# Performance work log

Measured on AMD Instinct MI355X. Metric: run time of the kernel, lower is better.

The kernel has to match this reference:

```python
import jax, jax.numpy as jnp
import jax.scipy as jsp
import numpy as np

NUM_EMBEDDINGS = 256
EMBEDDING_DIM = 64
SPARSITY_LEVEL = 4
N_BINS = 16
COEF_MAX = 3.0
COEF_MU = 50.0
COMMITMENT_COST = 0.25
EPSILON = 1e-10


def _normalize_dict(dictionary):
    # F.normalize(dict, p=2, dim=0, eps): x / max(||x||_2, eps) per column
    nrm = jnp.linalg.norm(dictionary, axis=0, keepdims=True)
    return dictionary / jnp.maximum(nrm, EPSILON)


def _quantize_coeff_mu_law(coeff):
    inv_log1p_mu = 1.0 / np.log1p(COEF_MU)  # scalar constant
    c = jnp.clip(coeff, -COEF_MAX, COEF_MAX) / COEF_MAX
    encoded = jnp.sign(c) * jnp.log1p(jnp.abs(c) * COEF_MU) * inv_log1p_mu
    scaled = (encoded + 1.0) * ((N_BINS - 1) / 2.0)
    bin_idx = jnp.clip(jnp.round(scaled).astype(jnp.int32), 0, N_BINS - 1)
    # dequantize
    z = bin_idx.astype(coeff.dtype) * (2.0 / (N_BINS - 1)) - 1.0
    decoded = jnp.sign(z) * (jnp.expm1(jnp.abs(z) / inv_log1p_mu) / COEF_MU) * COEF_MAX
    return bin_idx, decoded


def batch_omp_with_support(X, Dn, K):
    # X: [M, Bs] signals, Dn: [M, N] normalized dictionary
    G = Dn.T @ Dn                       # [N, N] Gram
    h_bar = (Dn.T @ X).T                # [Bs, N] correlations
    Bs, N = h_bar.shape
    dt = h_bar.dtype
    h = h_bar
    mask = jnp.zeros((Bs, N), dtype=bool)
    L = jnp.ones((Bs, 1, 1), dtype=dt)  # incremental Cholesky of G[I, I]
    I = jnp.zeros((Bs, 0), dtype=jnp.int32)
    x_sel = jnp.zeros((Bs, 0), dtype=dt)
    rows = jnp.arange(Bs)
    for k in range(1, K + 1):  # K is small & static -> unrolled
        idx = jnp.argmax(jnp.abs(h) * (~mask), axis=1).astype(jnp.int32)
        mask = mask.at[rows, idx].set(True)
        if k > 1:
            G_stack = G[I, idx[:, None]]                     # [Bs, k-1]
            w = jsp.linalg.solve_triangular(L, G_stack[..., None], lower=True)  # [Bs,k-1,1]
            wT = jnp.swapaxes(w, 1, 2)                       # [Bs,1,k-1]
            w_corner = jnp.sqrt(jnp.clip(1.0 - jnp.sum(wT * wT, axis=2, keepdims=True), 1e-12))
            top = jnp.concatenate([L, jnp.zeros((Bs, k - 1, 1), dt)], axis=2)
            bot = jnp.concatenate([wT, w_corner], axis=2)
            L = jnp.concatenate([top, bot], axis=1)          # [Bs,k,k]
        I = jnp.concatenate([I, idx[:, None]], axis=1)       # [Bs,k]
        h_stack = jnp.take_along_axis(h_bar, I, axis=1)[..., None]  # [Bs,k,1]
        # cholesky_solve: L L^T x = h
        y = jsp.linalg.solve_triangular(L, h_stack, lower=True)
        xs = jsp.linalg.solve_triangular(jnp.swapaxes(L, 1, 2), y, lower=False)
        x_sel = xs[..., 0]                                   # [Bs,k] coeffs aligned w/ support
        beta = jnp.einsum('bk,bkn->bn', x_sel, G[I])         # [Bs,N]
        h = h_bar - beta
    return I, x_sel


def setup_inputs() -> dict:
    key = jax.random.key(0)
    k1, k2 = jax.random.split(key)
    z_e = jax.random.normal(k1, (32, EMBEDDING_DIM, 64, 64), dtype=jnp.float32)
    dictionary = jax.random.normal(k2, (EMBEDDING_DIM, NUM_EMBEDDINGS), dtype=jnp.float32) * 0.02
    return {"z_e": z_e, "dictionary": dictionary}


def reference(z_e, dictionary):
    B, C, H, W = z_e.shape
    Dn = _normalize_dict(dictionary)
    signals = jnp.transpose(z_e, (0, 2, 3, 1)).reshape(-1, C).T  # [C, B*H*W]
    # OMP runs with no grad (torch.no_grad in original)
    support, coeffs = jax.lax.stop_gradient(
        batch_omp_with_support(jax.lax.stop_gradient(signals), jax.lax.stop_gradient(Dn), SPARSITY_LEVEL)
    )
    # mu-law quantize coefficients (constants w.r.t. grads)
    bin_idx, coeffs_q = _quantize_coeff_mu_law(coeffs)
    # reconstruct with quantized coeffs; dictionary path is differentiable
    atoms = Dn.T[support]                                    # [Bs, K, C]
    recon_flat = jnp.einsum('bkc,bk->bc', atoms, coeffs_q)
    recon = jnp.transpose(recon_flat.reshape(B, H, W, C), (0, 3, 1, 2))
    # VQ-VAE style losses + STE
    e_latent_loss = jnp.mean((jax.lax.stop_gradient(recon) - z_e) ** 2)
    q_latent_loss = jnp.mean((recon - jax.lax.stop_gradient(z_e)) ** 2)
    loss = q_latent_loss + COMMITMENT_COST * e_latent_loss
    z_q = z_e + jax.lax.stop_gradient(recon - z_e)
    return z_q, loss


if __name__ == '__main__':
    out = reference(**setup_inputs())
    print(out[0].shape, out[1])
```

## Files before the change

kernel.cpp:

```cpp
#include <hip/hip_runtime.h>
#include <math.h>

#define NEMB 256
#define DIM 64
#define SIGS_B 64
#define THREADS 256
#define NSIG 131072
#define GRID (NSIG / SIGS_B)

#define LOG1P50 3.9318256327243257
#define INV_MU_F ((float)(1.0 / LOG1P50))
#define TWO15_F ((float)(2.0 / 15.0))

#define LB_SIG   0
#define LB_XS    16384
#define LB_QI    17408
#define LB_RED   18432
#define LDS_BYTES 18464

typedef float f2 __attribute__((ext_vector_type(2)));

__device__ __forceinline__ float rdlane_f(float v, int lane)
{
    return __builtin_bit_cast(float, __builtin_amdgcn_readlane(__builtin_bit_cast(int, v), lane));
}

template<int CTRL>
__device__ __forceinline__ float dpp_fmax(float m)
{
    int sh = __builtin_amdgcn_update_dpp(0, __builtin_bit_cast(int, m), CTRL, 0xf, 0xf, true);
    return fmaxf(m, __builtin_bit_cast(float, sh));
}

__device__ __forceinline__ float wave_max_nn(float v)
{
    v = dpp_fmax<0x111>(v);
    v = dpp_fmax<0x112>(v);
    v = dpp_fmax<0x114>(v);
    v = dpp_fmax<0x118>(v);
    v = dpp_fmax<0x142>(v);
    v = dpp_fmax<0x143>(v);
    return v;
}

__global__ void k_ng(const float* __restrict__ D, float* __restrict__ Dn,
                     float* __restrict__ G,
                     double* __restrict__ loss_acc, unsigned int* __restrict__ ctr)
{
#pragma clang fp contract(off)
    __shared__ float nrmS[NEMB];
    __shared__ float coli[DIM];
    int i = blockIdx.x, j = threadIdx.x;
    if (i == 0 && j == 0) { loss_acc[0] = 0.0; ctr[0] = 0u; }
    float ss = 0.0f;
    for (int c = 0; c < DIM; c++) {
        float v = D[c * NEMB + j];
        float sq = v * v;
        ss = ss + sq;
    }
    float nrm = fmaxf(sqrtf(ss), 1e-10f);
    nrmS[j] = nrm;
    __syncthreads();
    if (j < DIM) {
        float dni = D[j * NEMB + i] / nrmS[i];
        coli[j] = dni;
        Dn[j * NEMB + i] = dni;
    }
    __syncthreads();
    float s = 0.0f;
#pragma unroll 8
    for (int c = 0; c < DIM; c++) {
        float dnj = D[c * NEMB + j] / nrm;
        s = fmaf(coli[c], dnj, s);
    }
    G[i * NEMB + j] = s;
}

__device__ __forceinline__ float quant_decode(float coeff)
{
#pragma clang fp contract(off)
    float c = fminf(fmaxf(coeff, -3.0f), 3.0f) / 3.0f;
    float ac = fabsf(c);
    float sgn = (c > 0.0f) ? 1.0f : ((c < 0.0f) ? -1.0f : 0.0f);
    float l = log1pf(ac * 50.0f);
    float enc = (sgn * l) * INV_MU_F;
    float scaled = (enc + 1.0f) * 7.5f;
    int bin = (int)rintf(scaled);
    bin = bin < 0 ? 0 : (bin > 15 ? 15 : bin);
    float t = (float)bin * TWO15_F;
    float zv = t - 1.0f;
    float az = fabsf(zv);
    float sz = (zv > 0.0f) ? 1.0f : ((zv < 0.0f) ? -1.0f : 0.0f);
    float e = expm1f(az / INV_MU_F);
    return (sz * (e / 50.0f)) * 3.0f;
}

__device__ __forceinline__ void omp_pair(const f2* hbA_in, const f2* hbB_in,
                                         int lane, int hi,
                                         const float* __restrict__ G,
                                         float* __restrict__ xsv,
                                         int* __restrict__ qi, int sA)
{
#pragma clang fp contract(off)
    f2 hbsiA[2] = {hbA_in[0], hbA_in[1]};
    f2 hbsiB[2] = {hbB_in[0], hbB_in[1]};
    f2 hA[2] = {hbsiA[0], hbsiA[1]};
    f2 hB[2] = {hbsiB[0], hbsiB[1]};
    f2 GrA[3][2], GrB[3][2];
    float Lm[4][4];
    int IvA[4], IvB[4];
    float y[4], xs[4];
    int m4A = 0, m4B = 0;
#pragma unroll
    for (int kk = 0; kk < 4; kk++) {
        float bvA = -1.0f, bvB = -1.0f;
        int bjA = 0, bjB = 0;
#pragma unroll
        for (int j = 0; j < 4; j++) {
            float vA_ = (m4A & (1 << j)) ? 0.0f : fabsf(hA[j >> 1][j & 1]);
            if (vA_ > bvA) { bvA = vA_; bjA = j; }
            float vB_ = (m4B & (1 << j)) ? 0.0f : fabsf(hB[j >> 1][j & 1]);
            if (vB_ > bvB) { bvB = vB_; bjB = j; }
        }
        float mA = wave_max_nn(bvA);
        float mB = wave_max_nn(bvB);
        float vmaxA = rdlane_f(mA, 63);
        float vmaxB = rdlane_f(mB, 63);
        unsigned long long ballA = __ballot(bvA == vmaxA);
        unsigned long long ballB = __ballot(bvB == vmaxB);
        int ownerA = __ffsll((long long)ballA) - 1;
        int ownerB = __ffsll((long long)ballB) - 1;
        int bjAo = __builtin_amdgcn_readlane(bjA, ownerA);
        int bjBo = __builtin_amdgcn_readlane(bjB, ownerB);
        int idxA = 4 * ownerA + bjAo;
        int idxB = 4 * ownerB + bjBo;
        m4A |= (lane == ownerA) ? (1 << bjAo) : 0;
        m4B |= (lane == ownerB) ? (1 << bjBo) : 0;
        IvA[kk] = idxA; IvB[kk] = idxB;
        float tvA = hbsiA[0][0];
        tvA = (bjA == 1) ? hbsiA[0][1] : tvA;
        tvA = (bjA == 2) ? hbsiA[1][0] : tvA;
        tvA = (bjA == 3) ? hbsiA[1][1] : tvA;
        float tvB = hbsiB[0][0];
        tvB = (bjB == 1) ? hbsiB[0][1] : tvB;
        tvB = (bjB == 2) ? hbsiB[1][0] : tvB;
        tvB = (bjB == 3) ? hbsiB[1][1] : tvB;
        float hselA = rdlane_f(tvA, ownerA);
        float hselB = rdlane_f(tvB, ownerB);
        float hsel = hi ? hselB : hselA;
        if (kk < 3) {
            const float4 ga = *(const float4*)(G + ((size_t)idxA << 8) + 4 * lane);
            const float4 gb = *(const float4*)(G + ((size_t)idxB << 8) + 4 * lane);
            GrA[kk][0].x = ga.x; GrA[kk][0].y = ga.y;
            GrA[kk][1].x = ga.z; GrA[kk][1].y = ga.w;
            GrB[kk][0].x = gb.x; GrB[kk][0].y = gb.y;
            GrB[kk][1].x = gb.z; GrB[kk][1].y = gb.w;
        }
        if (kk > 0) {
            float Gs[3], w[3];
#pragma unroll
            for (int j = 0; j < 3; j++)
                if (j < kk) {
                    float eA = GrA[j][0][0];
                    eA = (bjAo == 1) ? GrA[j][0][1] : eA;
                    eA = (bjAo == 2) ? GrA[j][1][0] : eA;
                    eA = (bjAo == 3) ? GrA[j][1][1] : eA;
                    float eB = GrB[j][0][0];
                    eB = (bjBo == 1) ? GrB[j][0][1] : eB;
                    eB = (bjBo == 2) ? GrB[j][1][0] : eB;
                    eB = (bjBo == 3) ? GrB[j][1][1] : eB;
                    float gA = rdlane_f(eA, ownerA);
                    float gB = rdlane_f(eB, ownerB);
                    Gs[j] = hi ? gB : gA;
                }
#pragma unroll
            for (int r = 0; r < 3; r++) {
                if (r < kk) {
                    float acc = 0.0f;
#pragma unroll
                    for (int cc = 0; cc < 3; cc++)
                        if (cc < r) { float p = Lm[r][cc] * w[cc]; acc = acc + p; }
                    float t2 = Gs[r] - acc;
                    w[r] = (r == 0) ? t2 : t2 / Lm[r][r];
                }
            }
            float ssum = 0.0f;
#pragma unroll
            for (int j = 0; j < 3; j++)
                if (j < kk) { float p = w[j] * w[j]; ssum = ssum + p; }
            float om = 1.0f - ssum;
            float wc = sqrtf(fmaxf(om, 1e-12f));
#pragma unroll
            for (int cc = 0; cc < 3; cc++)
                if (cc < kk) Lm[kk][cc] = w[cc];
            Lm[kk][kk] = wc;
        } else {
            Lm[0][0] = 1.0f;
        }
        {
            float acc = 0.0f;
#pragma unroll
            for (int cc = 0; cc < 3; cc++)
                if (cc < kk) { float p = Lm[kk][cc] * y[cc]; acc = acc + p; }
            float t2 = hsel - acc;
            y[kk] = (kk == 0) ? t2 : t2 / Lm[kk][kk];
        }
#pragma unroll
        for (int r = 3; r >= 0; r--) {
            if (r <= kk) {
                float acc = 0.0f;
#pragma unroll
                for (int cc = 0; cc < 4; cc++)
                    if (cc > r && cc <= kk) { float p = Lm[cc][r] * xs[cc]; acc = acc + p; }
                float t2 = y[r] - acc;
                xs[r] = (r == 0) ? t2 : t2 / Lm[r][r];
            }
        }
        if (kk < 3) {
            float xsA[4], xsB[4];
#pragma unroll
            for (int j = 0; j < 4; j++)
                if (j <= kk) {
                    xsA[j] = rdlane_f(xs[j], 0);
                    xsB[j] = rdlane_f(xs[j], 32);
                }
#pragma unroll
            for (int jp = 0; jp < 2; jp++) {
                f2 bsA = {0.0f, 0.0f};
                f2 bsB = {0.0f, 0.0f};
#pragma unroll
                for (int jj = 0; jj < 3; jj++)
                    if (jj <= kk) {
                        f2 xa = {xsA[jj], xsA[jj]};
                        f2 xb = {xsB[jj], xsB[jj]};
                        f2 pA = xa * GrA[jj][jp];
                        bsA = bsA + pA;
                        f2 pB = xb * GrB[jj][jp];
                        bsB = bsB + pB;
                    }
                hA[jp] = hbsiA[jp] - bsA;
                hB[jp] = hbsiB[jp] - bsB;
            }
        }
    }
    if ((lane & 31) == 0) {
        int s = sA + hi;
#pragma unroll
        for (int j = 0; j < 4; j++) {
            xsv[j * SIGS_B + s] = xs[j];
            qi[j * SIGS_B + s] = hi ? IvB[j] : IvA[j];
        }
    }
}

__launch_bounds__(THREADS, 4)
__global__ void k_omp(const float* __restrict__ z,
                      const float* __restrict__ Dn_g,
                      const float* __restrict__ G,
                      double* __restrict__ loss_acc,
                      unsigned int* __restrict__ ctr,
                      float* __restrict__ zq,
                      float* __restrict__ loss_out)
{
    extern __shared__ char smem[];
    float* sig = (float*)(smem + LB_SIG);
    float* xsv = (float*)(smem + LB_XS);
    int* qi = (int*)(smem + LB_QI);
    double* red = (double*)(smem + LB_RED);

    int tid = threadIdx.x;
    int lane = tid & 63;
    int hi = lane >> 5;
    int wid = tid >> 6;

    long sbase = (long)blockIdx.x * SIGS_B;
    int b = (int)(sbase >> 12);
    int pl0 = (int)(sbase & 4095);
    const float* zb = z + ((size_t)b << 18) + pl0;
    {
        int w = tid & (SIGS_B - 1);
        int g = tid >> 6;
#pragma unroll
        for (int i = 0; i < 16; i++) {
            int c = g * 16 + i;
            sig[c * SIGS_B + w] = zb[(size_t)c * 4096 + w];
        }
    }
    __syncthreads();

    for (int g2 = 0; g2 < 2; g2++) {
        int s0 = wid * 16 + g2 * 8;
        f2 hb[8][2];
#pragma unroll
        for (int a = 0; a < 8; a++) {
            hb[a][0] = (f2){0.0f, 0.0f};
            hb[a][1] = (f2){0.0f, 0.0f};
        }
#pragma unroll 8
        for (int c = 0; c < DIM; c++) {
            float4 sva = *(const float4*)(sig + c * SIGS_B + s0);
            float4 svb = *(const float4*)(sig + c * SIGS_B + s0 + 4);
            float s8[8] = {sva.x, sva.y, sva.z, sva.w, svb.x, svb.y, svb.z, svb.w};
            float4 dv = *(const float4*)(Dn_g + c * NEMB + 4 * lane);
            f2 d0; d0.x = dv.x; d0.y = dv.y;
            f2 d1; d1.x = dv.z; d1.y = dv.w;
#pragma unroll
            for (int a = 0; a < 8; a++) {
                f2 sa = {s8[a], s8[a]};
                hb[a][0] = __builtin_elementwise_fma(sa, d0, hb[a][0]);
                hb[a][1] = __builtin_elementwise_fma(sa, d1, hb[a][1]);
            }
        }
#pragma unroll
        for (int p = 0; p < 4; p++)
            omp_pair(hb[2 * p], hb[2 * p + 1], lane, hi, G, xsv, qi, s0 + 2 * p);
    }
    __syncthreads();

    {
        int jq = tid >> 6;
        int wq = tid & (SIGS_B - 1);
        xsv[jq * SIGS_B + wq] = quant_decode(xsv[jq * SIGS_B + wq]);
    }
    __syncthreads();

    double lsum = 0.0;
    float* zqb = zq + ((size_t)b << 18) + pl0;
    {
#pragma clang fp contract(off)
        int w = tid & (SIGS_B - 1);
        int g = tid >> 6;
        float q0 = xsv[0 * SIGS_B + w], q1 = xsv[1 * SIGS_B + w];
        float q2 = xsv[2 * SIGS_B + w], q3 = xsv[3 * SIGS_B + w];
        int i0 = qi[0 * SIGS_B + w], i1 = qi[1 * SIGS_B + w];
        int i2 = qi[2 * SIGS_B + w], i3 = qi[3 * SIGS_B + w];
#pragma unroll
        for (int ci = 0; ci < 16; ci++) {
            int c = g * 16 + ci;
            const float* dr = Dn_g + c * NEMB;
            float p0 = q0 * dr[i0];
            float p1 = q1 * dr[i1];
            float p2 = q2 * dr[i2];
            float p3 = q3 * dr[i3];
            float r = p0 + p1;
            r = r + p2;
            r = r + p3;
            float zev = sig[c * SIGS_B + w];
            float d = r - zev;
            float zqv = zev + d;
            lsum += (double)d * (double)d;
            zqb[(size_t)c * 4096 + w] = zqv;
        }
    }
#pragma unroll
    for (int off = 32; off > 0; off >>= 1) lsum += __shfl_xor(lsum, off);
    if (lane == 0) red[wid] = lsum;
    __syncthreads();
    if (tid == 0) {
        double t = 0.0;
#pragma unroll
        for (int i = 0; i < 4; i++) t += red[i];
        atomicAdd(loss_acc, t);
        __threadfence();
        unsigned int done = atomicAdd(ctr, 1u);
        if (done == GRID - 1) {
            double m = atomicAdd(loss_acc, 0.0) / 8388608.0;
            loss_out[0] = (float)(m + 0.25 * m);
        }
    }
}

extern "C" void kernel_launch(void* const* d_in, const int* in_sizes, int n_in,
                              void* d_out, int out_size, void* d_ws, size_t ws_size,
                              hipStream_t stream)
{
    const float* z = (const float*)d_in[0];
    const float* D = (const float*)d_in[1];
    float* out = (float*)d_out;
    char* ws = (char*)d_ws;
    double* loss_acc = (double*)ws;
    unsigned int* ctr = (unsigned int*)(ws + 8);
    float* Dn = (float*)(ws + 256);
    float* G = (float*)(ws + 256 + 65536);

    k_ng<<<NEMB, NEMB, 0, stream>>>(D, Dn, G, loss_acc, ctr);
    hipFuncSetAttribute(reinterpret_cast<const void*>(k_omp),
                        hipFuncAttributeMaxDynamicSharedMemorySize, LDS_BYTES);
    k_omp<<<GRID, THREADS, LDS_BYTES, stream>>>(z, Dn, G, loss_acc, ctr, out, out + 8388608);
    (void)in_sizes; (void)n_in; (void)out_size; (void)ws_size;
}
```

Before: 309.3 us.

## Run OMP on four signals per wave and gather reconstruction atoms from transposed dictionary

The OMP solve now processes four signals per wavefront, one per 16-lane quarter, instead of two per half-wave. The Cholesky update is written out with scalar registers, and the Gram entries it needs are read directly from global memory instead of being extracted from cached Gram rows with lane reads. The reconstruction step now reads atoms from a new transposed dictionary copy with float4 loads instead of strided scalar gathers. In exchange, the code carries more live registers and more redundant Gram row loads per iteration, which could hurt occupancy.

```diff
diff --git a/kernel.cpp b/kernel.cpp
--- a/kernel.cpp
+++ b/kernel.cpp
@@ -44,7 +44,7 @@
 }
 
 __global__ void k_ng(const float* __restrict__ D, float* __restrict__ Dn,
-                     float* __restrict__ G,
+                     float* __restrict__ DnT, float* __restrict__ G,
                      double* __restrict__ loss_acc, unsigned int* __restrict__ ctr)
 {
 #pragma clang fp contract(off)
@@ -65,6 +65,7 @@
         float dni = D[j * NEMB + i] / nrmS[i];
         coli[j] = dni;
         Dn[j * NEMB + i] = dni;
+        DnT[i * DIM + j] = dni;
     }
     __syncthreads();
     float s = 0.0f;
@@ -95,167 +96,238 @@
     return (sz * (e / 50.0f)) * 3.0f;
 }
 
-__device__ __forceinline__ void omp_pair(const f2* hbA_in, const f2* hbB_in,
-                                         int lane, int hi,
+__device__ __forceinline__ void omp_quad(const f2 (*hbsi)[2], int lane, int qt,
                                          const float* __restrict__ G,
                                          float* __restrict__ xsv,
-                                         int* __restrict__ qi, int sA)
+                                         int* __restrict__ qi, int s0)
 {
 #pragma clang fp contract(off)
-    f2 hbsiA[2] = {hbA_in[0], hbA_in[1]};
-    f2 hbsiB[2] = {hbB_in[0], hbB_in[1]};
-    f2 hA[2] = {hbsiA[0], hbsiA[1]};
-    f2 hB[2] = {hbsiB[0], hbsiB[1]};
-    f2 GrA[3][2], GrB[3][2];
-    float Lm[4][4];
-    int IvA[4], IvB[4];
-    float y[4], xs[4];
-    int m4A = 0, m4B = 0;
+    f2 h0[2] = {hbsi[0][0], hbsi[0][1]};
+    f2 h1[2] = {hbsi[1][0], hbsi[1][1]};
+    f2 h2[2] = {hbsi[2][0], hbsi[2][1]};
+    f2 h3[2] = {hbsi[3][0], hbsi[3][1]};
+    int m40 = 0, m41 = 0, m42 = 0, m43 = 0;
+    int Iv0[4], Iv1[4], Iv2[4], Iv3[4];
+    int Ivq[4];
+    float L10, L11, L20, L21, L22, L30, L31, L32, L33;
+    float y0, y1, y2, y3;
+    float x0 = 0.f, x1 = 0.f, x2 = 0.f, x3 = 0.f;
 #pragma unroll
     for (int kk = 0; kk < 4; kk++) {
-        float bvA = -1.0f, bvB = -1.0f;
-        int bjA = 0, bjB = 0;
+        float bv0 = -1.f, bv1 = -1.f, bv2 = -1.f, bv3 = -1.f;
+        int bj0 = 0, bj1 = 0, bj2 = 0, bj3 = 0;
 #pragma unroll
         for (int j = 0; j < 4; j++) {
-            float vA_ = (m4A & (1 << j)) ? 0.0f : fabsf(hA[j >> 1][j & 1]);
-            if (vA_ > bvA) { bvA = vA_; bjA = j; }
-            float vB_ = (m4B & (1 << j)) ? 0.0f : fabsf(hB[j >> 1][j & 1]);
-            if (vB_ > bvB) { bvB = vB_; bjB = j; }
-        }
-        float mA = wave_max_nn(bvA);
-        float mB = wave_max_nn(bvB);
-        float vmaxA = rdlane_f(mA, 63);
-        float vmaxB = rdlane_f(mB, 63);
-        unsigned long long ballA = __ballot(bvA == vmaxA);
-        unsigned long long ballB = __ballot(bvB == vmaxB);
-        int ownerA = __ffsll((long long)ballA) - 1;
-        int ownerB = __ffsll((long long)ballB) - 1;
-        int bjAo = __builtin_amdgcn_readlane(bjA, ownerA);
-        int bjBo = __builtin_amdgcn_readlane(bjB, ownerB);
-        int idxA = 4 * ownerA + bjAo;
-        int idxB = 4 * ownerB + bjBo;
-        m4A |= (lane == ownerA) ? (1 << bjAo) : 0;
-        m4B |= (lane == ownerB) ? (1 << bjBo) : 0;
-        IvA[kk] = idxA; IvB[kk] = idxB;
-        float tvA = hbsiA[0][0];
-        tvA = (bjA == 1) ? hbsiA[0][1] : tvA;
-        tvA = (bjA == 2) ? hbsiA[1][0] : tvA;
-        tvA = (bjA == 3) ? hbsiA[1][1] : tvA;
-        float tvB = hbsiB[0][0];
-        tvB = (bjB == 1) ? hbsiB[0][1] : tvB;
-        tvB = (bjB == 2) ? hbsiB[1][0] : tvB;
-        tvB = (bjB == 3) ? hbsiB[1][1] : tvB;
-        float hselA = rdlane_f(tvA, ownerA);
-        float hselB = rdlane_f(tvB, ownerB);
-        float hsel = hi ? hselB : hselA;
+            float a0 = (m40 & (1 << j)) ? 0.f : fabsf(h0[j >> 1][j & 1]);
+            if (a0 > bv0) { bv0 = a0; bj0 = j; }
+            float a1 = (m41 & (1 << j)) ? 0.f : fabsf(h1[j >> 1][j & 1]);
+            if (a1 > bv1) { bv1 = a1; bj1 = j; }
+            float a2 = (m42 & (1 << j)) ? 0.f : fabsf(h2[j >> 1][j & 1]);
+            if (a2 > bv2) { bv2 = a2; bj2 = j; }
+            float a3 = (m43 & (1 << j)) ? 0.f : fabsf(h3[j >> 1][j & 1]);
+            if (a3 > bv3) { bv3 = a3; bj3 = j; }
+        }
+        float r0 = wave_max_nn(bv0);
+        float r1 = wave_max_nn(bv1);
+        float r2 = wave_max_nn(bv2);
+        float r3 = wave_max_nn(bv3);
+        float vm0 = rdlane_f(r0, 63), vm1 = rdlane_f(r1, 63);
+        float vm2 = rdlane_f(r2, 63), vm3 = rdlane_f(r3, 63);
+        unsigned long long bl0 = __ballot(bv0 == vm0);
+        unsigned long long bl1 = __ballot(bv1 == vm1);
+        unsigned long long bl2 = __ballot(bv2 == vm2);
+        unsigned long long bl3 = __ballot(bv3 == vm3);
+        int ow0 = __ffsll((long long)bl0) - 1;
+        int ow1 = __ffsll((long long)bl1) - 1;
+        int ow2 = __ffsll((long long)bl2) - 1;
+        int ow3 = __ffsll((long long)bl3) - 1;
+        int bo0 = __builtin_amdgcn_readlane(bj0, ow0);
+        int bo1 = __builtin_amdgcn_readlane(bj1, ow1);
+        int bo2 = __builtin_amdgcn_readlane(bj2, ow2);
+        int bo3 = __builtin_amdgcn_readlane(bj3, ow3);
+        int id0 = 4 * ow0 + bo0;
+        int id1 = 4 * ow1 + bo1;
+        int id2 = 4 * ow2 + bo2;
+        int id3 = 4 * ow3 + bo3;
+        m40 |= (lane == ow0) ? (1 << bo0) : 0;
+        m41 |= (lane == ow1) ? (1 << bo1) : 0;
+        m42 |= (lane == ow2) ? (1 << bo2) : 0;
+        m43 |= (lane == ow3) ? (1 << bo3) : 0;
+        float tv0 = hbsi[0][0][0];
+        tv0 = (bj0 == 1) ? hbsi[0][0][1] : tv0;
+        tv0 = (bj0 == 2) ? hbsi[0][1][0] : tv0;
+        tv0 = (bj0 == 3) ? hbsi[0][1][1] : tv0;
+        float tv1 = hbsi[1][0][0];
+        tv1 = (bj1 == 1) ? hbsi[1][0][1] : tv1;
+        tv1 = (bj1 == 2) ? hbsi[1][1][0] : tv1;
+        tv1 = (bj1 == 3) ? hbsi[1][1][1] : tv1;
+        float tv2 = hbsi[2][0][0];
+        tv2 = (bj2 == 1) ? hbsi[2][0][1] : tv2;
+        tv2 = (bj2 == 2) ? hbsi[2][1][0] : tv2;
+        tv2 = (bj2 == 3) ? hbsi[2][1][1] : tv2;
+        float tv3 = hbsi[3][0][0];
+        tv3 = (bj3 == 1) ? hbsi[3][0][1] : tv3;
+        tv3 = (bj3 == 2) ? hbsi[3][1][0] : tv3;
+        tv3 = (bj3 == 3) ? hbsi[3][1][1] : tv3;
+        float hs0 = rdlane_f(tv0, ow0);
+        float hs1 = rdlane_f(tv1, ow1);
+        float hs2 = rdlane_f(tv2, ow2);
+        float hs3 = rdlane_f(tv3, ow3);
+        Iv0[kk] = id0; Iv1[kk] = id1; Iv2[kk] = id2; Iv3[kk] = id3;
+        float hsel = (qt & 2) ? ((qt & 1) ? hs3 : hs2) : ((qt & 1) ? hs1 : hs0);
+        int idxq = (qt & 2) ? ((qt & 1) ? id3 : id2) : ((qt & 1) ? id1 : id0);
+        Ivq[kk] = idxq;
+        float Gs0 = 0.f, Gs1 = 0.f, Gs2 = 0.f;
+        if (kk > 0) Gs0 = G[(size_t)(Ivq[0] << 8) + idxq];
+        if (kk > 1) Gs1 = G[(size_t)(Ivq[1] << 8) + idxq];
+        if (kk > 2) Gs2 = G[(size_t)(Ivq[2] << 8) + idxq];
+        if (kk == 1) {
+            float cw0 = Gs0;
+            float css = cw0 * cw0;
+            float om = 1.0f - css;
+            L10 = cw0;
+            L11 = sqrtf(fmaxf(om, 1e-12f));
+        }
+        if (kk == 2) {
+            float cw0 = Gs0;
+            float ct = Gs1 - L10 * cw0;
+            float cw1 = ct / L11;
+            float css = cw0 * cw0;
+            float cp = cw1 * cw1; css = css + cp;
+            float om = 1.0f - css;
+            L20 = cw0; L21 = cw1;
+            L22 = sqrtf(fmaxf(om, 1e-12f));
+        }
+        if (kk == 3) {
+            float cw0 = Gs0;
+            float ct = Gs1 - L10 * cw0;
+            float cw1 = ct / L11;
+            float ca = L20 * cw0;
+            float cp = L21 * cw1; ca = ca + cp;
+            float ct3 = Gs2 - ca;
+            float cw2 = ct3 / L22;
+            float css = cw0 * cw0;
+            cp = cw1 * cw1; css = css + cp;
+            cp = cw2 * cw2; css = css + cp;
+            float om = 1.0f - css;
+            L30 = cw0; L31 = cw1; L32 = cw2;
+            L33 = sqrtf(fmaxf(om, 1e-12f));
+        }
+        if (kk == 0) y0 = hsel;
+        if (kk == 1) { float a = L10 * y0; y1 = (hsel - a) / L11; }
+        if (kk == 2) { float a = L20 * y0; float p = L21 * y1; a = a + p;
+                       y2 = (hsel - a) / L22; }
+        if (kk == 3) { float a = L30 * y0; float p = L31 * y1; a = a + p;
+                       p = L32 * y2; a = a + p;
+                       y3 = (hsel - a) / L33; }
+        if (kk == 0) { x0 = y0; }
+        if (kk == 1) {
+            x1 = y1 / L11;
+            float a = L10 * x1;
+            x0 = y0 - a;
+        }
+        if (kk == 2) {
+            x2 = y2 / L22;
+            float a = L21 * x2;
+            x1 = (y1 - a) / L11;
+            a = L10 * x1;
+            float p = L20 * x2; a = a + p;
+            x0 = y0 - a;
+        }
+        if (kk == 3) {
+            x3 = y3 / L33;
+            float a = L32 * x3;
+            x2 = (y2 - a) / L22;
+            a = L21 * x2;
+            float p = L31 * x3; a = a + p;
+            x1 = (y1 - a) / L11;
+            a = L10 * x1;
+            p = L20 * x2; a = a + p;
+            p = L30 * x3; a = a + p;
+            x0 = y0 - a;
+        }
         if (kk < 3) {
-            const float4 ga = *(const float4*)(G + ((size_t)idxA << 8) + 4 * lane);
-            const float4 gb = *(const float4*)(G + ((size_t)idxB << 8) + 4 * lane);
-            GrA[kk][0].x = ga.x; GrA[kk][0].y = ga.y;
-            GrA[kk][1].x = ga.z; GrA[kk][1].y = ga.w;
-            GrB[kk][0].x = gb.x; GrB[kk][0].y = gb.y;
-            GrB[kk][1].x = gb.z; GrB[kk][1].y = gb.w;
-        }
-        if (kk > 0) {
-            float Gs[3], w[3];
-#pragma unroll
-            for (int j = 0; j < 3; j++)
-                if (j < kk) {
-                    float eA = GrA[j][0][0];
-                    eA = (bjAo == 1) ? GrA[j][0][1] : eA;
-                    eA = (bjAo == 2) ? GrA[j][1][0] : eA;
-                    eA = (bjAo == 3) ? GrA[j][1][1] : eA;
-                    float eB = GrB[j][0][0];
-                    eB = (bjBo == 1) ? GrB[j][0][1] : eB;
-                    eB = (bjBo == 2) ? GrB[j][1][0] : eB;
-                    eB = (bjBo == 3) ? GrB[j][1][1] : eB;
-                    float gA = rdlane_f(eA, ownerA);
-                    float gB = rdlane_f(eB, ownerB);
-                    Gs[j] = hi ? gB : gA;
-                }
-#pragma unroll
-            for (int r = 0; r < 3; r++) {
-                if (r < kk) {
-                    float acc = 0.0f;
-#pragma unroll
-                    for (int cc = 0; cc < 3; cc++)
-                        if (cc < r) { float p = Lm[r][cc] * w[cc]; acc = acc + p; }
-                    float t2 = Gs[r] - acc;
-                    w[r] = (r == 0) ? t2 : t2 / Lm[r][r];
-                }
-            }
-            float ssum = 0.0f;
-#pragma unroll
-            for (int j = 0; j < 3; j++)
-                if (j < kk) { float p = w[j] * w[j]; ssum = ssum + p; }
-            float om = 1.0f - ssum;
-            float wc = sqrtf(fmaxf(om, 1e-12f));
-#pragma unroll
-            for (int cc = 0; cc < 3; cc++)
-                if (cc < kk) Lm[kk][cc] = w[cc];
-            Lm[kk][kk] = wc;
-        } else {
-            Lm[0][0] = 1.0f;
-        }
-        {
-            float acc = 0.0f;
-#pragma unroll
-            for (int cc = 0; cc < 3; cc++)
-                if (cc < kk) { float p = Lm[kk][cc] * y[cc]; acc = acc + p; }
-            float t2 = hsel - acc;
-            y[kk] = (kk == 0) ? t2 : t2 / Lm[kk][kk];
-        }
-#pragma unroll
-        for (int r = 3; r >= 0; r--) {
-            if (r <= kk) {
-                float acc = 0.0f;
-#pragma unroll
-                for (int cc = 0; cc < 4; cc++)
-                    if (cc > r && cc <= kk) { float p = Lm[cc][r] * xs[cc]; acc = acc + p; }
-                float t2 = y[r] - acc;
-                xs[r] = (r == 0) ? t2 : t2 / Lm[r][r];
-            }
-        }
-        if (kk < 3) {
-            float xsA[4], xsB[4];
-#pragma unroll
-            for (int j = 0; j < 4; j++)
-                if (j <= kk) {
-                    xsA[j] = rdlane_f(xs[j], 0);
-                    xsB[j] = rdlane_f(xs[j], 32);
-                }
-#pragma unroll
-            for (int jp = 0; jp < 2; jp++) {
-                f2 bsA = {0.0f, 0.0f};
-                f2 bsB = {0.0f, 0.0f};
-#pragma unroll
-                for (int jj = 0; jj < 3; jj++)
-                    if (jj <= kk) {
-                        f2 xa = {xsA[jj], xsA[jj]};
-                        f2 xb = {xsB[jj], xsB[jj]};
-                        f2 pA = xa * GrA[jj][jp];
-                        bsA = bsA + pA;
-                        f2 pB = xb * GrB[jj][jp];
-                        bsB = bsB + pB;
-                    }
-                hA[jp] = hbsiA[jp] - bsA;
-                hB[jp] = hbsiB[jp] - bsB;
-            }
-        }
-    }
-    if ((lane & 31) == 0) {
-        int s = sA + hi;
-#pragma unroll
-        for (int j = 0; j < 4; j++) {
-            xsv[j * SIGS_B + s] = xs[j];
-            qi[j * SIGS_B + s] = hi ? IvB[j] : IvA[j];
-        }
+            float xb00 = rdlane_f(x0, 0),  xb10 = rdlane_f(x0, 16);
+            float xb20 = rdlane_f(x0, 32), xb30 = rdlane_f(x0, 48);
+            float xb01 = 0.f, xb11 = 0.f, xb21 = 0.f, xb31 = 0.f;
+            float xb02 = 0.f, xb12 = 0.f, xb22 = 0.f, xb32 = 0.f;
+            if (kk > 0) { xb01 = rdlane_f(x1, 0);  xb11 = rdlane_f(x1, 16);
+                          xb21 = rdlane_f(x1, 32); xb31 = rdlane_f(x1, 48); }
+            if (kk > 1) { xb02 = rdlane_f(x2, 0);  xb12 = rdlane_f(x2, 16);
+                          xb22 = rdlane_f(x2, 32); xb32 = rdlane_f(x2, 48); }
+            const int l4 = 4 * lane;
+            float4 R00 = *(const float4*)(G + ((size_t)Iv0[0] << 8) + l4);
+            float4 R10 = *(const float4*)(G + ((size_t)Iv1[0] << 8) + l4);
+            float4 R20 = *(const float4*)(G + ((size_t)Iv2[0] << 8) + l4);
+            float4 R30 = *(const float4*)(G + ((size_t)Iv3[0] << 8) + l4);
+            float4 R01, R11, R21, R31, R02, R12, R22, R32;
+            if (kk > 0) {
+                R01 = *(const float4*)(G + ((size_t)Iv0[1] << 8) + l4);
+                R11 = *(const float4*)(G + ((size_t)Iv1[1] << 8) + l4);
+                R21 = *(const float4*)(G + ((size_t)Iv2[1] << 8) + l4);
+                R31 = *(const float4*)(G + ((size_t)Iv3[1] << 8) + l4);
+            }
+            if (kk > 1) {
+                R02 = *(const float4*)(G + ((size_t)Iv0[2] << 8) + l4);
+                R12 = *(const float4*)(G + ((size_t)Iv1[2] << 8) + l4);
+                R22 = *(const float4*)(G + ((size_t)Iv2[2] << 8) + l4);
+                R32 = *(const float4*)(G + ((size_t)Iv3[2] << 8) + l4);
+            }
+            {
+                f2 bsa = (f2){xb00, xb00} * (f2){R00.x, R00.y};
+                f2 bsb = (f2){xb00, xb00} * (f2){R00.z, R00.w};
+                if (kk > 0) { f2 pa = (f2){xb01, xb01} * (f2){R01.x, R01.y}; bsa = bsa + pa;
+                              f2 pb = (f2){xb01, xb01} * (f2){R01.z, R01.w}; bsb = bsb + pb; }
+                if (kk > 1) { f2 pa = (f2){xb02, xb02} * (f2){R02.x, R02.y}; bsa = bsa + pa;
+                              f2 pb = (f2){xb02, xb02} * (f2){R02.z, R02.w}; bsb = bsb + pb; }
+                h0[0] = hbsi[0][0] - bsa;
+                h0[1] = hbsi[0][1] - bsb;
+            }
+            {
+                f2 bsa = (f2){xb10, xb10} * (f2){R10.x, R10.y};
+                f2 bsb = (f2){xb10, xb10} * (f2){R10.z, R10.w};
+                if (kk > 0) { f2 pa = (f2){xb11, xb11} * (f2){R11.x, R11.y}; bsa = bsa + pa;
+                              f2 pb = (f2){xb11, xb11} * (f2){R11.z, R11.w}; bsb = bsb + pb; }
+                if (kk > 1) { f2 pa = (f2){xb12, xb12} * (f2){R12.x, R12.y}; bsa = bsa + pa;
+                              f2 pb = (f2){xb12, xb12} * (f2){R12.z, R12.w}; bsb = bsb + pb; }
+                h1[0] = hbsi[1][0] - bsa;
+                h1[1] = hbsi[1][1] - bsb;
+            }
+            {
+                f2 bsa = (f2){xb20, xb20} * (f2){R20.x, R20.y};
+                f2 bsb = (f2){xb20, xb20} * (f2){R20.z, R20.w};
+                if (kk > 0) { f2 pa = (f2){xb21, xb21} * (f2){R21.x, R21.y}; bsa = bsa + pa;
+                              f2 pb = (f2){xb21, xb21} * (f2){R21.z, R21.w}; bsb = bsb + pb; }
+                if (kk > 1) { f2 pa = (f2){xb22, xb22} * (f2){R22.x, R22.y}; bsa = bsa + pa;
+                              f2 pb = (f2){xb22, xb22} * (f2){R22.z, R22.w}; bsb = bsb + pb; }
+                h2[0] = hbsi[2][0] - bsa;
+                h2[1] = hbsi[2][1] - bsb;
+            }
+            {
+                f2 bsa = (f2){xb30, xb30} * (f2){R30.x, R30.y};
+                f2 bsb = (f2){xb30, xb30} * (f2){R30.z, R30.w};
+                if (kk > 0) { f2 pa = (f2){xb31, xb31} * (f2){R31.x, R31.y}; bsa = bsa + pa;
+                              f2 pb = (f2){xb31, xb31} * (f2){R31.z, R31.w}; bsb = bsb + pb; }
+                if (kk > 1) { f2 pa = (f2){xb32, xb32} * (f2){R32.x, R32.y}; bsa = bsa + pa;
+                              f2 pb = (f2){xb32, xb32} * (f2){R32.z, R32.w}; bsb = bsb + pb; }
+                h3[0] = hbsi[3][0] - bsa;
+                h3[1] = hbsi[3][1] - bsb;
+            }
+        }
+    }
+    if ((lane & 15) == 0) {
+        int s = s0 + qt;
+        xsv[0 * SIGS_B + s] = x0; xsv[1 * SIGS_B + s] = x1;
+        xsv[2 * SIGS_B + s] = x2; xsv[3 * SIGS_B + s] = x3;
+        qi[0 * SIGS_B + s] = Ivq[0]; qi[1 * SIGS_B + s] = Ivq[1];
+        qi[2 * SIGS_B + s] = Ivq[2]; qi[3 * SIGS_B + s] = Ivq[3];
     }
 }
 
 __launch_bounds__(THREADS, 4)
 __global__ void k_omp(const float* __restrict__ z,
                       const float* __restrict__ Dn_g,
+                      const float* __restrict__ DnT_g,
                       const float* __restrict__ G,
                       double* __restrict__ loss_acc,
                       unsigned int* __restrict__ ctr,
@@ -270,7 +342,7 @@
 
     int tid = threadIdx.x;
     int lane = tid & 63;
-    int hi = lane >> 5;
+    int qt = lane >> 4;
     int wid = tid >> 6;
 
     long sbase = (long)blockIdx.x * SIGS_B;
@@ -311,9 +383,8 @@
                 hb[a][1] = __builtin_elementwise_fma(sa, d1, hb[a][1]);
             }
         }
-#pragma unroll
-        for (int p = 0; p < 4; p++)
-            omp_pair(hb[2 * p], hb[2 * p + 1], lane, hi, G, xsv, qi, s0 + 2 * p);
+        omp_quad(hb,     lane, qt, G, xsv, qi, s0);
+        omp_quad(hb + 4, lane, qt, G, xsv, qi, s0 + 4);
     }
     __syncthreads();
 
@@ -334,22 +405,36 @@
         float q2 = xsv[2 * SIGS_B + w], q3 = xsv[3 * SIGS_B + w];
         int i0 = qi[0 * SIGS_B + w], i1 = qi[1 * SIGS_B + w];
         int i2 = qi[2 * SIGS_B + w], i3 = qi[3 * SIGS_B + w];
-#pragma unroll
-        for (int ci = 0; ci < 16; ci++) {
-            int c = g * 16 + ci;
-            const float* dr = Dn_g + c * NEMB;
-            float p0 = q0 * dr[i0];
-            float p1 = q1 * dr[i1];
-            float p2 = q2 * dr[i2];
-            float p3 = q3 * dr[i3];
-            float r = p0 + p1;
-            r = r + p2;
-            r = r + p3;
-            float zev = sig[c * SIGS_B + w];
-            float d = r - zev;
-            float zqv = zev + d;
-            lsum += (double)d * (double)d;
-            zqb[(size_t)c * 4096 + w] = zqv;
+        const float* t0p = DnT_g + (i0 << 6) + (g << 4);
+        const float* t1p = DnT_g + (i1 << 6) + (g << 4);
+        const float* t2p = DnT_g + (i2 << 6) + (g << 4);
+        const float* t3p = DnT_g + (i3 << 6) + (g << 4);
+#pragma unroll
+        for (int cb = 0; cb < 4; cb++) {
+            float4 d0 = *(const float4*)(t0p + 4 * cb);
+            float4 d1 = *(const float4*)(t1p + 4 * cb);
+            float4 d2 = *(const float4*)(t2p + 4 * cb);
+            float4 d3 = *(const float4*)(t3p + 4 * cb);
+#pragma unroll
+            for (int u = 0; u < 4; u++) {
+                int c = (g << 4) + (cb << 2) + u;
+                float e0 = (u == 0) ? d0.x : (u == 1) ? d0.y : (u == 2) ? d0.z : d0.w;
+                float e1 = (u == 0) ? d1.x : (u == 1) ? d1.y : (u == 2) ? d1.z : d1.w;
+                float e2 = (u == 0) ? d2.x : (u == 1) ? d2.y : (u == 2) ? d2.z : d2.w;
+                float e3 = (u == 0) ? d3.x : (u == 1) ? d3.y : (u == 2) ? d3.z : d3.w;
+                float p0 = q0 * e0;
+                float p1 = q1 * e1;
+                float p2 = q2 * e2;
+                float p3 = q3 * e3;
+                float r = p0 + p1;
+                r = r + p2;
+                r = r + p3;
+                float zev = sig[c * SIGS_B + w];
+                float d = r - zev;
+                float zqv = zev + d;
+                lsum += (double)d * (double)d;
+                zqb[(size_t)c * 4096 + w] = zqv;
+            }
         }
     }
 #pragma unroll
@@ -382,10 +467,11 @@
     unsigned int* ctr = (unsigned int*)(ws + 8);
     float* Dn = (float*)(ws + 256);
     float* G = (float*)(ws + 256 + 65536);
-
-    k_ng<<<NEMB, NEMB, 0, stream>>>(D, Dn, G, loss_acc, ctr);
+    float* DnT = (float*)(ws + 256 + 65536 + 262144);
+
+    k_ng<<<NEMB, NEMB, 0, stream>>>(D, Dn, DnT, G, loss_acc, ctr);
     hipFuncSetAttribute(reinterpret_cast<const void*>(k_omp),
                         hipFuncAttributeMaxDynamicSharedMemorySize, LDS_BYTES);
-    k_omp<<<GRID, THREADS, LDS_BYTES, stream>>>(z, Dn, G, loss_acc, ctr, out, out + 8388608);
+    k_omp<<<GRID, THREADS, LDS_BYTES, stream>>>(z, Dn, DnT, G, loss_acc, ctr, out, out + 8388608);
     (void)in_sizes; (void)n_in; (void)out_size; (void)ws_size;
 }
```

Measured after the change: 299.5 us. 1.03x faster.
